# Optimization experiments

Hardware: AMD Instinct MI355X
Metric: run time of the kernel (lower is better)

Reference implementation:

```python
import jax, jax.numpy as jnp
import numpy as np

N_NODES = 100000
N_EDGES = 1600000
D_IN = 128
D_HID = 128
D_OUT = 128


def setup_inputs() -> dict:
    key = jax.random.key(0)
    ks = jax.random.split(key, 8)
    x = jax.random.normal(ks[0], (N_NODES, D_IN), dtype=jnp.float32)
    edge_index = jax.random.randint(ks[1], (2, N_EDGES), 0, N_NODES, dtype=jnp.int64)
    # GraphConv layer 1: lin_rel (with bias) applied to aggregated messages, lin_root (no bias) to x
    s1 = 1.0 / np.sqrt(D_IN)
    W1_rel = jax.random.uniform(ks[2], (D_IN, D_HID), jnp.float32, -s1, s1)
    b1 = jax.random.uniform(ks[3], (D_HID,), jnp.float32, -s1, s1)
    W1_root = jax.random.uniform(ks[4], (D_IN, D_HID), jnp.float32, -s1, s1)
    s2 = 1.0 / np.sqrt(D_HID)
    W2_rel = jax.random.uniform(ks[5], (D_HID, D_OUT), jnp.float32, -s2, s2)
    b2 = jax.random.uniform(ks[6], (D_OUT,), jnp.float32, -s2, s2)
    W2_root = jax.random.uniform(ks[7], (D_HID, D_OUT), jnp.float32, -s2, s2)
    return {"x": x, "edge_index": edge_index, "W1_rel": W1_rel, "b1": b1,
            "W1_root": W1_root, "W2_rel": W2_rel, "b2": b2, "W2_root": W2_root}


def graph_conv(x, src, dst, W_rel, b, W_root, n_nodes):
    # PyG GraphConv (aggr='add'): out_i = W_rel @ sum_{j->i} x_j + b + W_root @ x_i
    msgs = jnp.take(x, src, axis=0)                       # [E, F] gather
    agg = jax.ops.segment_sum(msgs, dst, num_segments=n_nodes)  # [N, F] scatter-add
    return agg @ W_rel + b + x @ W_root


def reference(x, edge_index, W1_rel, b1, W1_root, W2_rel, b2, W2_root):
    src, dst = edge_index[0], edge_index[1]
    n = x.shape[0]
    h = graph_conv(x, src, dst, W1_rel, b1, W1_root, n)
    h = jax.nn.relu(h)
    out = graph_conv(h, src, dst, W2_rel, b2, W2_root, n)
    return out
```

## Files before the change

### kernel.cpp

```cpp
#include <hip/hip_runtime.h>

#define D 128
#define TILE_R 32
#define LDS_STRIDE 260
#define GBM 64
#define APAD 264

#define NB 512
#define NPB 256
#define EPB_A 2048

typedef __attribute__((ext_vector_type(8))) short bf16x8;
typedef __attribute__((ext_vector_type(4))) float f32x4;

static __device__ __forceinline__ ushort f2b(float f) {
    union { float f; uint u; } v; v.f = f;
    uint r = (v.u + 0x7FFFu + ((v.u >> 16) & 1u)) >> 16;
    return (ushort)r;
}
static __device__ __forceinline__ float blo(uint u) {
    union { uint u; float f; } v; v.u = u << 16; return v.f;
}
static __device__ __forceinline__ float bhi(uint u) {
    union { uint u; float f; } v; v.u = u & 0xFFFF0000u; return v.f;
}


__global__ __launch_bounds__(256) void bucket_count_kernel(
    const int* __restrict__ dst, int* __restrict__ bcnt, int nedges)
{
    __shared__ int h[NB];
    int t = threadIdx.x;
    for (int i = t; i < NB; i += 256) h[i] = 0;
    __syncthreads();
    int base = blockIdx.x * EPB_A;
    #pragma unroll
    for (int i = 0; i < 8; ++i) {
        int e = base + i * 256 + t;
        if (e < nedges) atomicAdd(&h[dst[e] >> 8], 1);
    }
    __syncthreads();
    for (int i = t; i < NB; i += 256) if (h[i]) atomicAdd(&bcnt[i], h[i]);
}

__global__ __launch_bounds__(512) void bucket_scan_kernel(
    const int* __restrict__ bcnt, int* __restrict__ bbase, int* __restrict__ bcur)
{
    __shared__ int sh[NB];
    int t = threadIdx.x;
    int v = bcnt[t];
    sh[t] = v; __syncthreads();
    int val = v;
    for (int off = 1; off < NB; off <<= 1) {
        int u = (t >= off) ? sh[t - off] : 0;
        __syncthreads();
        val += u; sh[t] = val; __syncthreads();
    }
    int excl = val - v;
    bbase[t] = excl;
    bcur[t] = excl;
}

__global__ __launch_bounds__(256) void bucket_scatter_kernel(
    const int* __restrict__ src, const int* __restrict__ dst,
    int* __restrict__ bcur, uint* __restrict__ ebuf, int nedges)
{
    __shared__ int h[NB];
    __shared__ int res[NB];
    int t = threadIdx.x;
    for (int i = t; i < NB; i += 256) h[i] = 0;
    __syncthreads();
    int base = blockIdx.x * EPB_A;
    int d[8], s[8], bkt[8];
    #pragma unroll
    for (int i = 0; i < 8; ++i) {
        int e = base + i * 256 + t;
        if (e < nedges) {
            d[i] = dst[e]; s[i] = src[e]; bkt[i] = d[i] >> 8;
            atomicAdd(&h[bkt[i]], 1);
        } else bkt[i] = -1;
    }
    __syncthreads();
    for (int i = t; i < NB; i += 256) {
        int c = h[i];
        res[i] = c ? atomicAdd(&bcur[i], c) : 0;
    }
    __syncthreads();
    #pragma unroll
    for (int i = 0; i < 8; ++i) {
        if (bkt[i] >= 0) {
            int pos = atomicAdd(&res[bkt[i]], 1);
            ebuf[pos] = ((uint)(d[i] & (NPB - 1)) << 17) | (uint)s[i];
        }
    }
}

__global__ __launch_bounds__(256) void csr_finalize_kernel(
    const uint* __restrict__ ebuf, const int* __restrict__ bbase,
    const int* __restrict__ bcnt, int* __restrict__ csr_src,
    int* __restrict__ ends, int n)
{
    __shared__ int cnt[NPB];
    __shared__ int cur[NPB];
    __shared__ int sh[NPB];
    int b = blockIdx.x, t = threadIdx.x;
    int ebase = bbase[b];
    int ecnt = bcnt[b];
    cnt[t] = 0;
    __syncthreads();
    for (int i = t; i < ecnt; i += 256)
        atomicAdd(&cnt[ebuf[ebase + i] >> 17], 1);
    __syncthreads();
    int v = cnt[t];
    sh[t] = v; __syncthreads();
    int val = v;
    for (int off = 1; off < 256; off <<= 1) {
        int u = (t >= off) ? sh[t - off] : 0;
        __syncthreads();
        val += u; sh[t] = val; __syncthreads();
    }
    int node = b * NPB + t;
    if (node < n) ends[node] = ebase + val;
    cur[t] = ebase + (val - v);
    __syncthreads();
    for (int i = t; i < ecnt; i += 256) {
        uint p = ebuf[ebase + i];
        int pos = atomicAdd(&cur[p >> 17], 1);
        csr_src[pos] = (int)(p & 0x1FFFFu);
    }
}


__global__ __launch_bounds__(256) void conv_f32_bf16_kernel(
    const float* __restrict__ in, ushort* __restrict__ out, int n8)
{
    int i = blockIdx.x * 256 + threadIdx.x;
    if (i >= n8) return;
    float4 a = reinterpret_cast<const float4*>(in)[i * 2];
    float4 b = reinterpret_cast<const float4*>(in)[i * 2 + 1];
    uint4 r;
    r.x = f2b(a.x) | ((uint)f2b(a.y) << 16);
    r.y = f2b(a.z) | ((uint)f2b(a.w) << 16);
    r.z = f2b(b.x) | ((uint)f2b(b.y) << 16);
    r.w = f2b(b.z) | ((uint)f2b(b.w) << 16);
    reinterpret_cast<uint4*>(out)[i] = r;
}

__global__ __launch_bounds__(256) void wt_kernel(
    const float* __restrict__ Wrel, const float* __restrict__ Wroot,
    ushort* __restrict__ Wt)
{
    int idx = blockIdx.x * 256 + threadIdx.x;
    int n = idx >> 8, k = idx & 255;
    float v = (k < 128) ? Wrel[(size_t)k * D + n] : Wroot[(size_t)(k - 128) * D + n];
    Wt[idx] = f2b(v);
}

__global__ __launch_bounds__(256) void layer_fused_kernel(
    const ushort* __restrict__ feat, const int* __restrict__ csr_src,
    const int* __restrict__ ends, const ushort* __restrict__ Wt,
    const float* __restrict__ bias, float* outf, ushort* outb,
    int n, int mode)
{
    __shared__ ushort As[GBM * APAD];
    const int t = threadIdx.x;
    const int wave = t >> 6, lane = t & 63;
    const int base = blockIdx.x * GBM;

    #pragma unroll
    for (int m = 0; m < 4; ++m) {
        int q = t + m * 256;
        int r = q >> 4, c = q & 15;
        int row = base + r;
        uint4 v = make_uint4(0, 0, 0, 0);
        if (row < n) v = reinterpret_cast<const uint4*>(feat + (size_t)row * D)[c];
        *reinterpret_cast<uint4*>(&As[r * APAD + 128 + c * 8]) = v;
    }

    {
        const int g = t >> 4, l = t & 15;
        #pragma unroll 1
        for (int sub = 0; sub < 4; ++sub) {
            int r = g * 4 + sub;
            int node = base + r;
            float a0=0,a1=0,a2=0,a3=0,a4=0,a5=0,a6=0,a7=0;
            float c0=0,c1=0,c2=0,c3=0,c4=0,c5=0,c6=0,c7=0;
            if (node < n) {
                int jb = (node == 0) ? 0 : ends[node - 1];
                int je = ends[node];
                int j = jb;
                for (; j + 2 <= je; j += 2) {
                    int s0 = csr_src[j], s1 = csr_src[j + 1];
                    uint4 v0 = reinterpret_cast<const uint4*>(feat + (size_t)s0 * D)[l];
                    uint4 v1 = reinterpret_cast<const uint4*>(feat + (size_t)s1 * D)[l];
                    a0 += blo(v0.x); a1 += bhi(v0.x); a2 += blo(v0.y); a3 += bhi(v0.y);
                    a4 += blo(v0.z); a5 += bhi(v0.z); a6 += blo(v0.w); a7 += bhi(v0.w);
                    c0 += blo(v1.x); c1 += bhi(v1.x); c2 += blo(v1.y); c3 += bhi(v1.y);
                    c4 += blo(v1.z); c5 += bhi(v1.z); c6 += blo(v1.w); c7 += bhi(v1.w);
                }
                if (j < je) {
                    int s0 = csr_src[j];
                    uint4 v0 = reinterpret_cast<const uint4*>(feat + (size_t)s0 * D)[l];
                    a0 += blo(v0.x); a1 += bhi(v0.x); a2 += blo(v0.y); a3 += bhi(v0.y);
                    a4 += blo(v0.z); a5 += bhi(v0.z); a6 += blo(v0.w); a7 += bhi(v0.w);
                }
            }
            uint4 rp;
            rp.x = f2b(a0 + c0) | ((uint)f2b(a1 + c1) << 16);
            rp.y = f2b(a2 + c2) | ((uint)f2b(a3 + c3) << 16);
            rp.z = f2b(a4 + c4) | ((uint)f2b(a5 + c5) << 16);
            rp.w = f2b(a6 + c6) | ((uint)f2b(a7 + c7) << 16);
            *reinterpret_cast<uint4*>(&As[r * APAD + l * 8]) = rp;
        }
    }
    __syncthreads();

    const int bcol0 = wave * 32;
    const int l15 = lane & 15;
    f32x4 acc[4][2];
    #pragma unroll
    for (int rt = 0; rt < 4; ++rt)
        #pragma unroll
        for (int nt = 0; nt < 2; ++nt) acc[rt][nt] = (f32x4){0.f, 0.f, 0.f, 0.f};

    #pragma unroll 1
    for (int ks = 0; ks < 8; ++ks) {
        const int kk = ks * 32 + (lane >> 4) * 8;
        bf16x8 a0_ = *reinterpret_cast<const bf16x8*>(&As[(l15 +  0) * APAD + kk]);
        bf16x8 a1_ = *reinterpret_cast<const bf16x8*>(&As[(l15 + 16) * APAD + kk]);
        bf16x8 a2_ = *reinterpret_cast<const bf16x8*>(&As[(l15 + 32) * APAD + kk]);
        bf16x8 a3_ = *reinterpret_cast<const bf16x8*>(&As[(l15 + 48) * APAD + kk]);
        bf16x8 b0_ = *reinterpret_cast<const bf16x8*>(Wt + (size_t)(bcol0 + l15) * 256 + kk);
        bf16x8 b1_ = *reinterpret_cast<const bf16x8*>(Wt + (size_t)(bcol0 + 16 + l15) * 256 + kk);
        acc[0][0] = __builtin_amdgcn_mfma_f32_16x16x32_bf16(a0_, b0_, acc[0][0], 0, 0, 0);
        acc[0][1] = __builtin_amdgcn_mfma_f32_16x16x32_bf16(a0_, b1_, acc[0][1], 0, 0, 0);
        acc[1][0] = __builtin_amdgcn_mfma_f32_16x16x32_bf16(a1_, b0_, acc[1][0], 0, 0, 0);
        acc[1][1] = __builtin_amdgcn_mfma_f32_16x16x32_bf16(a1_, b1_, acc[1][1], 0, 0, 0);
        acc[2][0] = __builtin_amdgcn_mfma_f32_16x16x32_bf16(a2_, b0_, acc[2][0], 0, 0, 0);
        acc[2][1] = __builtin_amdgcn_mfma_f32_16x16x32_bf16(a2_, b1_, acc[2][1], 0, 0, 0);
        acc[3][0] = __builtin_amdgcn_mfma_f32_16x16x32_bf16(a3_, b0_, acc[3][0], 0, 0, 0);
        acc[3][1] = __builtin_amdgcn_mfma_f32_16x16x32_bf16(a3_, b1_, acc[3][1], 0, 0, 0);
    }

    #pragma unroll
    for (int rt = 0; rt < 4; ++rt)
        #pragma unroll
        for (int nt = 0; nt < 2; ++nt) {
            int col = bcol0 + nt * 16 + l15;
            float bv = bias[col];
            #pragma unroll
            for (int r = 0; r < 4; ++r) {
                int row = base + rt * 16 + (lane >> 4) * 4 + r;
                if (row >= n) continue;
                float v = acc[rt][nt][r] + bv;
                if (mode == 0) {
                    v = fmaxf(v, 0.f);
                    outb[(size_t)row * D + col] = f2b(v);
                } else {
                    outf[(size_t)row * D + col] = v;
                }
            }
        }
}


__global__ __launch_bounds__(256) void scatter_add_kernel(
    const float* __restrict__ feat, const int* __restrict__ src,
    const int* __restrict__ dst, float* agg, int nedges)
{
    int tid = blockIdx.x * 256 + threadIdx.x;
    int e = tid >> 5;
    if (e >= nedges) return;
    int l = tid & 31;
    int s = src[e];
    int d = dst[e];
    const float4 v = *reinterpret_cast<const float4*>(feat + (size_t)s * D + l * 4);
    float* o = agg + (size_t)d * D + l * 4;
    unsafeAtomicAdd(o + 0, v.x);
    unsafeAtomicAdd(o + 1, v.y);
    unsafeAtomicAdd(o + 2, v.z);
    unsafeAtomicAdd(o + 3, v.w);
}

__global__ __launch_bounds__(256) void gemm_fused_kernel(
    const float* __restrict__ A1, const float* A2,
    const float* __restrict__ Wrel, const float* __restrict__ Wroot,
    const float* __restrict__ bias, float* out, int n, int do_relu)
{
    __shared__ float Asf[TILE_R * LDS_STRIDE];
    const int t = threadIdx.x;
    const int base = blockIdx.x * TILE_R;

    #pragma unroll
    for (int m = 0; m < 8; ++m) {
        int q = t + m * 256;
        int r = q >> 6;
        int kk = (q & 63) << 2;
        int row = base + r;
        float4 v = make_float4(0.f, 0.f, 0.f, 0.f);
        if (row < n) {
            const float* p = (kk < 128) ? (A1 + (size_t)row * D + kk)
                                        : (A2 + (size_t)row * D + (kk - 128));
            v = *reinterpret_cast<const float4*>(p);
        }
        *reinterpret_cast<float4*>(&Asf[r * LDS_STRIDE + kk]) = v;
    }
    __syncthreads();

    const int rg = t >> 5;
    const int c0 = (t & 31) << 2;

    float acc[4][4];
    #pragma unroll
    for (int i = 0; i < 4; ++i)
        #pragma unroll
        for (int j = 0; j < 4; ++j) acc[i][j] = 0.f;

    const float* Wmats[2] = {Wrel, Wroot};
    #pragma unroll
    for (int half = 0; half < 2; ++half) {
        const float* W = Wmats[half];
        const int kb = half * 128;
        for (int k = 0; k < 128; k += 4) {
            float w[4][4];
            #pragma unroll
            for (int kk = 0; kk < 4; ++kk) {
                float4 wv = *reinterpret_cast<const float4*>(W + (size_t)(k + kk) * D + c0);
                w[kk][0] = wv.x; w[kk][1] = wv.y; w[kk][2] = wv.z; w[kk][3] = wv.w;
            }
            #pragma unroll
            for (int i = 0; i < 4; ++i) {
                float4 av = *reinterpret_cast<const float4*>(&Asf[(rg * 4 + i) * LDS_STRIDE + kb + k]);
                float a[4] = {av.x, av.y, av.z, av.w};
                #pragma unroll
                for (int kk = 0; kk < 4; ++kk)
                    #pragma unroll
                    for (int j = 0; j < 4; ++j)
                        acc[i][j] = fmaf(a[kk], w[kk][j], acc[i][j]);
            }
        }
    }

    float4 bv = *reinterpret_cast<const float4*>(bias + c0);
    float b[4] = {bv.x, bv.y, bv.z, bv.w};
    #pragma unroll
    for (int i = 0; i < 4; ++i) {
        int row = base + rg * 4 + i;
        if (row >= n) continue;
        float o[4];
        #pragma unroll
        for (int j = 0; j < 4; ++j) {
            float v = acc[i][j] + b[j];
            if (do_relu) v = fmaxf(v, 0.f);
            o[j] = v;
        }
        *reinterpret_cast<float4*>(out + (size_t)row * D + c0) =
            make_float4(o[0], o[1], o[2], o[3]);
    }
}

extern "C" void kernel_launch(void* const* d_in, const int* in_sizes, int n_in,
                              void* d_out, int out_size, void* d_ws, size_t ws_size,
                              hipStream_t stream) {
    const float* x       = (const float*)d_in[0];
    const int*   ei      = (const int*)d_in[1];
    const float* W1_rel  = (const float*)d_in[2];
    const float* b1      = (const float*)d_in[3];
    const float* W1_root = (const float*)d_in[4];
    const float* W2_rel  = (const float*)d_in[5];
    const float* b2      = (const float*)d_in[6];
    const float* W2_root = (const float*)d_in[7];
    float* out = (float*)d_out;

    const int E = in_sizes[1] / 2;
    const int N = in_sizes[0] / D;
    const int* src = ei;
    const int* dst = ei + E;

    size_t hbB   = ((size_t)N * D * 2 + 255) & ~(size_t)255;
    size_t xbB   = ((size_t)N * D * 2 + 255) & ~(size_t)255;
    size_t csrB  = ((size_t)E * 4 + 255) & ~(size_t)255;
    size_t endB  = ((size_t)(N + 1) * 4 + 255) & ~(size_t)255;
    size_t bktB  = ((size_t)(3 * NB + 8) * 4 + 255) & ~(size_t)255;
    size_t wtB   = (size_t)128 * 256 * 2;
    size_t need = hbB + xbB + csrB + endB + bktB + 2 * wtB;

    bool pack_ok = (N <= 131072) && ((size_t)E * 4 <= hbB);

    if (ws_size >= need && pack_ok) {
        char* w = (char*)d_ws;
        ushort* hb      = (ushort*)w;            w += hbB;
        ushort* xb      = (ushort*)w;            w += xbB;
        int*    csr_src = (int*)w;               w += csrB;
        int*    ends    = (int*)w;               w += endB;
        int*    bcnt    = (int*)w;
        int*    bbase   = bcnt + NB;
        int*    bcur    = bbase + NB;            w += bktB;
        ushort* Wt1     = (ushort*)w;            w += wtB;
        ushort* Wt2     = (ushort*)w;
        uint*   ebuf    = (uint*)hb;

        const int aBlocks = (E + EPB_A - 1) / EPB_A;
        const int nbu = (N + NPB - 1) / NPB;

        hipMemsetAsync(bcnt, 0, NB * sizeof(int), stream);
        bucket_count_kernel<<<aBlocks, 256, 0, stream>>>(dst, bcnt, E);
        bucket_scan_kernel<<<1, NB, 0, stream>>>(bcnt, bbase, bcur);
        bucket_scatter_kernel<<<aBlocks, 256, 0, stream>>>(src, dst, bcur, ebuf, E);
        csr_finalize_kernel<<<nbu, 256, 0, stream>>>(ebuf, bbase, bcnt, csr_src, ends, N);

        int n8 = N * D / 8;
        conv_f32_bf16_kernel<<<(n8 + 255) / 256, 256, 0, stream>>>(x, xb, n8);
        wt_kernel<<<128, 256, 0, stream>>>(W1_rel, W1_root, Wt1);
        wt_kernel<<<128, 256, 0, stream>>>(W2_rel, W2_root, Wt2);

        int layerBlocks = (N + GBM - 1) / GBM;

        layer_fused_kernel<<<layerBlocks, 256, 0, stream>>>(
            xb, csr_src, ends, Wt1, b1, nullptr, hb, N, 0);
        layer_fused_kernel<<<layerBlocks, 256, 0, stream>>>(
            hb, csr_src, ends, Wt2, b2, out, nullptr, N, 1);
    } else {
        float* agg = (float*)d_ws;
        size_t aggBytes = (size_t)N * D * sizeof(float);
        int scatterBlocks = (E * 32 + 255) / 256;
        int gemmBlocks = (N + TILE_R - 1) / TILE_R;
        hipMemsetAsync(agg, 0, aggBytes, stream);
        scatter_add_kernel<<<scatterBlocks, 256, 0, stream>>>(x, src, dst, agg, E);
        gemm_fused_kernel<<<gemmBlocks, 256, 0, stream>>>(agg, x, W1_rel, W1_root, b1, out, N, 1);
        hipMemsetAsync(agg, 0, aggBytes, stream);
        scatter_add_kernel<<<scatterBlocks, 256, 0, stream>>>(out, src, dst, agg, E);
        gemm_fused_kernel<<<gemmBlocks, 256, 0, stream>>>(agg, out, W2_rel, W2_root, b2, out, N, 0);
    }
}
```

Measured before the change: 292.7 us.

## Merge prep kernels into one launch and unroll edge gather by four

Folds the fp32-to-bf16 conversion of x, both weight transposes and the bucket-count pass into one heterogeneous prep kernel dispatched by block index. This removes three kernel launches and lets these independent jobs run concurrently. The per-node neighbor gather now issues four row loads per iteration instead of two, with four accumulator sets, to expose more memory-level parallelism. Occupancy is hinted with launch_bounds(256,4). The extra accumulators raise register pressure, and the occupancy hint may force spills.

```diff
diff --git a/kernel.cpp b/kernel.cpp
--- a/kernel.cpp
+++ b/kernel.cpp
@@ -25,23 +25,52 @@
     union { uint u; float f; } v; v.u = u & 0xFFFF0000u; return v.f;
 }
 
-
-__global__ __launch_bounds__(256) void bucket_count_kernel(
-    const int* __restrict__ dst, int* __restrict__ bcnt, int nedges)
+__global__ __launch_bounds__(256) void prep_kernel(
+    const float* __restrict__ x, ushort* __restrict__ xb, int n8,
+    const float* __restrict__ W1rel, const float* __restrict__ W1root, ushort* __restrict__ Wt1,
+    const float* __restrict__ W2rel, const float* __restrict__ W2root, ushort* __restrict__ Wt2,
+    const int* __restrict__ dst, int* __restrict__ bcnt, int nedges,
+    int nConvBlocks, int nCountBlocks)
 {
     __shared__ int h[NB];
-    int t = threadIdx.x;
-    for (int i = t; i < NB; i += 256) h[i] = 0;
-    __syncthreads();
-    int base = blockIdx.x * EPB_A;
-    #pragma unroll
-    for (int i = 0; i < 8; ++i) {
-        int e = base + i * 256 + t;
-        if (e < nedges) atomicAdd(&h[dst[e] >> 8], 1);
-    }
-    __syncthreads();
-    for (int i = t; i < NB; i += 256) if (h[i]) atomicAdd(&bcnt[i], h[i]);
-}
+    const int b = blockIdx.x, t = threadIdx.x;
+
+    if (b < nConvBlocks) {
+        int i = b * 256 + t;
+        if (i >= n8) return;
+        float4 a = reinterpret_cast<const float4*>(x)[i * 2];
+        float4 c = reinterpret_cast<const float4*>(x)[i * 2 + 1];
+        uint4 r;
+        r.x = f2b(a.x) | ((uint)f2b(a.y) << 16);
+        r.y = f2b(a.z) | ((uint)f2b(a.w) << 16);
+        r.z = f2b(c.x) | ((uint)f2b(c.y) << 16);
+        r.w = f2b(c.z) | ((uint)f2b(c.w) << 16);
+        reinterpret_cast<uint4*>(xb)[i] = r;
+    } else if (b < nConvBlocks + 256) {
+        int wb = b - nConvBlocks;
+        const float* Wrel  = (wb < 128) ? W1rel  : W2rel;
+        const float* Wroot = (wb < 128) ? W1root : W2root;
+        ushort* Wt = (wb < 128) ? Wt1 : Wt2;
+        int idx = (wb & 127) * 256 + t;
+        int n = idx >> 8, k = idx & 255;
+        float v = (k < 128) ? Wrel[(size_t)k * D + n] : Wroot[(size_t)(k - 128) * D + n];
+        Wt[idx] = f2b(v);
+    } else {
+        int cb = b - nConvBlocks - 256;
+        if (cb >= nCountBlocks) return;
+        for (int i = t; i < NB; i += 256) h[i] = 0;
+        __syncthreads();
+        int base = cb * EPB_A;
+        #pragma unroll
+        for (int i = 0; i < 8; ++i) {
+            int e = base + i * 256 + t;
+            if (e < nedges) atomicAdd(&h[dst[e] >> 8], 1);
+        }
+        __syncthreads();
+        for (int i = t; i < NB; i += 256) if (h[i]) atomicAdd(&bcnt[i], h[i]);
+    }
+}
+
 
 __global__ __launch_bounds__(512) void bucket_scan_kernel(
     const int* __restrict__ bcnt, int* __restrict__ bbase, int* __restrict__ bcur)
@@ -130,33 +159,7 @@
     }
 }
 
-
-__global__ __launch_bounds__(256) void conv_f32_bf16_kernel(
-    const float* __restrict__ in, ushort* __restrict__ out, int n8)
-{
-    int i = blockIdx.x * 256 + threadIdx.x;
-    if (i >= n8) return;
-    float4 a = reinterpret_cast<const float4*>(in)[i * 2];
-    float4 b = reinterpret_cast<const float4*>(in)[i * 2 + 1];
-    uint4 r;
-    r.x = f2b(a.x) | ((uint)f2b(a.y) << 16);
-    r.y = f2b(a.z) | ((uint)f2b(a.w) << 16);
-    r.z = f2b(b.x) | ((uint)f2b(b.y) << 16);
-    r.w = f2b(b.z) | ((uint)f2b(b.w) << 16);
-    reinterpret_cast<uint4*>(out)[i] = r;
-}
-
-__global__ __launch_bounds__(256) void wt_kernel(
-    const float* __restrict__ Wrel, const float* __restrict__ Wroot,
-    ushort* __restrict__ Wt)
-{
-    int idx = blockIdx.x * 256 + threadIdx.x;
-    int n = idx >> 8, k = idx & 255;
-    float v = (k < 128) ? Wrel[(size_t)k * D + n] : Wroot[(size_t)(k - 128) * D + n];
-    Wt[idx] = f2b(v);
-}
-
-__global__ __launch_bounds__(256) void layer_fused_kernel(
+__global__ __launch_bounds__(256, 4) void layer_fused_kernel(
     const ushort* __restrict__ feat, const int* __restrict__ csr_src,
     const int* __restrict__ ends, const ushort* __restrict__ Wt,
     const float* __restrict__ bias, float* outf, ushort* outb,
@@ -166,6 +169,7 @@
     const int t = threadIdx.x;
     const int wave = t >> 6, lane = t & 63;
     const int base = blockIdx.x * GBM;
+    const int l15 = lane & 15;
 
     #pragma unroll
     for (int m = 0; m < 4; ++m) {
@@ -185,20 +189,29 @@
             int node = base + r;
             float a0=0,a1=0,a2=0,a3=0,a4=0,a5=0,a6=0,a7=0;
             float c0=0,c1=0,c2=0,c3=0,c4=0,c5=0,c6=0,c7=0;
+            float e0=0,e1=0,e2=0,e3=0,e4=0,e5=0,e6=0,e7=0;
+            float g0=0,g1=0,g2=0,g3=0,g4=0,g5=0,g6=0,g7=0;
             if (node < n) {
                 int jb = (node == 0) ? 0 : ends[node - 1];
                 int je = ends[node];
                 int j = jb;
-                for (; j + 2 <= je; j += 2) {
+                for (; j + 4 <= je; j += 4) {
                     int s0 = csr_src[j], s1 = csr_src[j + 1];
+                    int s2 = csr_src[j + 2], s3 = csr_src[j + 3];
                     uint4 v0 = reinterpret_cast<const uint4*>(feat + (size_t)s0 * D)[l];
                     uint4 v1 = reinterpret_cast<const uint4*>(feat + (size_t)s1 * D)[l];
+                    uint4 v2 = reinterpret_cast<const uint4*>(feat + (size_t)s2 * D)[l];
+                    uint4 v3 = reinterpret_cast<const uint4*>(feat + (size_t)s3 * D)[l];
                     a0 += blo(v0.x); a1 += bhi(v0.x); a2 += blo(v0.y); a3 += bhi(v0.y);
                     a4 += blo(v0.z); a5 += bhi(v0.z); a6 += blo(v0.w); a7 += bhi(v0.w);
                     c0 += blo(v1.x); c1 += bhi(v1.x); c2 += blo(v1.y); c3 += bhi(v1.y);
                     c4 += blo(v1.z); c5 += bhi(v1.z); c6 += blo(v1.w); c7 += bhi(v1.w);
+                    e0 += blo(v2.x); e1 += bhi(v2.x); e2 += blo(v2.y); e3 += bhi(v2.y);
+                    e4 += blo(v2.z); e5 += bhi(v2.z); e6 += blo(v2.w); e7 += bhi(v2.w);
+                    g0 += blo(v3.x); g1 += bhi(v3.x); g2 += blo(v3.y); g3 += bhi(v3.y);
+                    g4 += blo(v3.z); g5 += bhi(v3.z); g6 += blo(v3.w); g7 += bhi(v3.w);
                 }
-                if (j < je) {
+                for (; j < je; ++j) {
                     int s0 = csr_src[j];
                     uint4 v0 = reinterpret_cast<const uint4*>(feat + (size_t)s0 * D)[l];
                     a0 += blo(v0.x); a1 += bhi(v0.x); a2 += blo(v0.y); a3 += bhi(v0.y);
@@ -206,17 +219,16 @@
                 }
             }
             uint4 rp;
-            rp.x = f2b(a0 + c0) | ((uint)f2b(a1 + c1) << 16);
-            rp.y = f2b(a2 + c2) | ((uint)f2b(a3 + c3) << 16);
-            rp.z = f2b(a4 + c4) | ((uint)f2b(a5 + c5) << 16);
-            rp.w = f2b(a6 + c6) | ((uint)f2b(a7 + c7) << 16);
+            rp.x = f2b(a0 + c0 + e0 + g0) | ((uint)f2b(a1 + c1 + e1 + g1) << 16);
+            rp.y = f2b(a2 + c2 + e2 + g2) | ((uint)f2b(a3 + c3 + e3 + g3) << 16);
+            rp.z = f2b(a4 + c4 + e4 + g4) | ((uint)f2b(a5 + c5 + e5 + g5) << 16);
+            rp.w = f2b(a6 + c6 + e6 + g6) | ((uint)f2b(a7 + c7 + e7 + g7) << 16);
             *reinterpret_cast<uint4*>(&As[r * APAD + l * 8]) = rp;
         }
     }
     __syncthreads();
 
     const int bcol0 = wave * 32;
-    const int l15 = lane & 15;
     f32x4 acc[4][2];
     #pragma unroll
     for (int rt = 0; rt < 4; ++rt)
@@ -402,17 +414,17 @@
 
         const int aBlocks = (E + EPB_A - 1) / EPB_A;
         const int nbu = (N + NPB - 1) / NPB;
+        const int n8 = N * D / 8;
+        const int nConvBlocks = (n8 + 255) / 256;
 
         hipMemsetAsync(bcnt, 0, NB * sizeof(int), stream);
-        bucket_count_kernel<<<aBlocks, 256, 0, stream>>>(dst, bcnt, E);
+        prep_kernel<<<nConvBlocks + 256 + aBlocks, 256, 0, stream>>>(
+            x, xb, n8, W1_rel, W1_root, Wt1, W2_rel, W2_root, Wt2,
+            dst, bcnt, E, nConvBlocks, aBlocks);
+
         bucket_scan_kernel<<<1, NB, 0, stream>>>(bcnt, bbase, bcur);
         bucket_scatter_kernel<<<aBlocks, 256, 0, stream>>>(src, dst, bcur, ebuf, E);
         csr_finalize_kernel<<<nbu, 256, 0, stream>>>(ebuf, bbase, bcnt, csr_src, ends, N);
-
-        int n8 = N * D / 8;
-        conv_f32_bf16_kernel<<<(n8 + 255) / 256, 256, 0, stream>>>(x, xb, n8);
-        wt_kernel<<<128, 256, 0, stream>>>(W1_rel, W1_root, Wt1);
-        wt_kernel<<<128, 256, 0, stream>>>(W2_rel, W2_root, Wt2);
 
         int layerBlocks = (N + GBM - 1) / GBM;
 
```

Result: faster. 262.5 us (-10.3%).
